# Kernel optimization log

Measured on AMD Instinct MI355X. Metric: run time of the kernel, lower is better.

Reference implementation:

```python
import jax, jax.numpy as jnp
import numpy as np

TWO_PI = 2.0 * np.pi
EPS = 1e-08


def setup_inputs() -> dict:
    key = jax.random.key(0)
    k1, k2, k3 = jax.random.split(key, 3)
    N, D = 1048576, 64
    samples = jax.random.normal(k1, (N, D), dtype=jnp.float32)
    Phi = jax.random.uniform(k2, (1,), dtype=jnp.float32)
    # mu init in torch: 2*rand - 0.5
    mu = 2.0 * jax.random.uniform(k3, (D,), dtype=jnp.float32) - 0.5
    Sigma = jnp.eye(D, dtype=jnp.float32)
    return {"samples": samples, "Phi": Phi, "mu": mu, "Sigma": Sigma}


def reference(samples, Phi, mu, Sigma):
    # Batched Mahalanobis quadratic form replacing the per-sample Python loop.
    inv_sigma = jnp.linalg.pinv(Sigma)                      # [D, D]
    det_sigma = jnp.linalg.det(Sigma)                       # scalar
    diff = samples - mu                                     # [N, D]
    # q_n = diff_n^T inv_sigma diff_n
    q = jnp.einsum('nd,de,ne->n', diff, inv_sigma, diff)    # [N]
    dens = Phi[0] * jnp.exp(-0.5 * q) / jnp.sqrt(TWO_PI * det_sigma)
    return -jnp.log(dens + EPS)                             # with_log=True path
```

## Files before the change

### kernel.cpp

```cpp
#include <hip/hip_runtime.h>


typedef __attribute__((ext_vector_type(8))) short s8bf;
typedef __attribute__((ext_vector_type(4))) float v4f;

#define TWO_PI_F 6.2831853071795864769f

__device__ __forceinline__ float bf2f(ushort u) {
    union { float f; unsigned int i; } v; v.i = ((unsigned int)u) << 16; return v.f;
}
__device__ __forceinline__ ushort f2bf(float f) {
    unsigned int x = __float_as_uint(f);
    return (ushort)((x + 0x7fffu + ((x >> 16) & 1u)) >> 16);
}
__device__ __forceinline__ s8bf pack8(float4 a, float4 b) {
    s8bf r;
    r[0] = (short)f2bf(a.x); r[1] = (short)f2bf(a.y);
    r[2] = (short)f2bf(a.z); r[3] = (short)f2bf(a.w);
    r[4] = (short)f2bf(b.x); r[5] = (short)f2bf(b.y);
    r[6] = (short)f2bf(b.z); r[7] = (short)f2bf(b.w);
    return r;
}

__global__ __launch_bounds__(256) void prep_kernel(const void* __restrict__ Sigma,
                                                   const void* __restrict__ Phi,
                                                   const void* __restrict__ mu,
                                                   void* __restrict__ ws) {
    __shared__ __align__(16) float colbuf[64];
    __shared__ __align__(16) float rowbuf[64];
    __shared__ __align__(16) float sA[64 * 65];
    __shared__ float smu[64];
    const int t = threadIdx.x;
    const int j = t & 63, w = t >> 6;
    const unsigned int wd0 = *(const unsigned int*)Sigma;
    const bool isf32 = (wd0 == 0x3F800000u);

    float ar[16];
    if (isf32) {
        const float* S = (const float*)Sigma;
#pragma unroll
        for (int ii = 0; ii < 16; ++ii) ar[ii] = S[(16 * w + ii) * 64 + j];
    } else {
        const ushort* S = (const ushort*)Sigma;
#pragma unroll
        for (int ii = 0; ii < 16; ++ii) ar[ii] = bf2f(S[(16 * w + ii) * 64 + j]);
    }
    if (t < 64) smu[t] = isf32 ? ((const float*)mu)[t] : bf2f(((const ushort*)mu)[t]);

    float det = 1.0f;
    for (int k = 0; k < 64; ++k) {
        if (j == k) {
#pragma unroll
            for (int ii = 0; ii < 16; ++ii) colbuf[16 * w + ii] = ar[ii];
        }
        if (w == (k >> 4)) {
            float val = ar[0];
#pragma unroll
            for (int ii = 1; ii < 16; ++ii) val = (ii == (k & 15)) ? ar[ii] : val;
            rowbuf[j] = val;
        }
        __syncthreads();
        const float piv = rowbuf[k];
        const float ip = 1.0f / piv;
        const float rk = rowbuf[j] * ip;
        det *= piv;
        const bool jk = (j == k);
#pragma unroll
        for (int ii = 0; ii < 16; ++ii) {
            float f = colbuf[16 * w + ii];
            float nv = fmaf(-f, rk, ar[ii]);
            nv = jk ? (-f * ip) : nv;
            if (16 * w + ii == k) nv = jk ? ip : rk;
            ar[ii] = nv;
        }
        __syncthreads();
    }

    ushort* wb = (ushort*)ws;
#pragma unroll
    for (int ii = 0; ii < 16; ++ii) wb[(16 * w + ii) * 64 + j] = f2bf(ar[ii]);
#pragma unroll
    for (int ii = 0; ii < 16; ++ii) sA[(16 * w + ii) * 65 + j] = ar[ii];
    __syncthreads();

    float* wf = (float*)((char*)ws + 8192);
    if (t < 64) {
        float dot = 0.0f;
#pragma unroll
        for (int jj = 0; jj < 64; ++jj) dot = fmaf(sA[t * 65 + jj], smu[jj], dot);
        wf[t] = 2.0f * dot;
        float pc = smu[t] * dot;
#pragma unroll
        for (int off = 1; off < 64; off <<= 1) pc += __shfl_xor(pc, off, 64);
        if (t == 0) {
            float ph = isf32 ? ((const float*)Phi)[0] : bf2f(((const ushort*)Phi)[0]);
            wf[64] = pc;
            wf[65] = ph / sqrtf(TWO_PI_F * det);
            wf[66] = isf32 ? 1.0f : 0.0f;
        }
    }
}

__global__ __launch_bounds__(256) void gmm_kernel(const void* __restrict__ Xv,
                                                  const void* __restrict__ ws,
                                                  void* __restrict__ outv,
                                                  int ntiles) {
    __shared__ __align__(16) ushort sB[64 * 72];
    __shared__ __align__(16) ushort sX[64 * 64];
    const int t = threadIdx.x;
    const int w = t >> 6, l = t & 63, n = l & 15, q = l >> 4;

    const ushort* wb = (const ushort*)ws;
#pragma unroll
    for (int p0 = 0; p0 < 2; ++p0) {
        int idx = p0 * 2048 + t * 8;
        int r = idx >> 6, c = idx & 63;
        *(uint4*)(&sB[r * 72 + c]) = *(const uint4*)(wb + idx);
    }
    const float* wf = (const float*)((const char*)ws + 8192);
    float vneg[4];
#pragma unroll
    for (int c = 0; c < 4; ++c) vneg[c] = -wf[c * 16 + n];
    const float c0 = wf[64], sc = wf[65];
    const bool isf32 = (wf[66] != 0.0f);
    __syncthreads();

    s8bf bfr[2][4];
#pragma unroll
    for (int s = 0; s < 2; ++s)
#pragma unroll
        for (int c = 0; c < 4; ++c)
            bfr[s][c] = *(const s8bf*)(&sB[(c * 16 + n) * 72 + s * 32 + q * 8]);

    const int sr = t >> 2, h = t & 3;
    const int c0i = 2 * h, c1i = 2 * h + 1;
    ushort* dst0 = sX + sr * 64 + ((c0i ^ (sr & 7)) * 8);
    ushort* dst1 = sX + sr * 64 + ((c1i ^ (sr & 7)) * 8);

    for (int tile = blockIdx.x; tile < ntiles; tile += gridDim.x) {
        s8bf ch0, ch1;
        if (isf32) {
            const float* src = (const float*)Xv + (size_t)tile * 4096 + sr * 64 + h * 16;
            float4 f0 = ((const float4*)src)[0];
            float4 f1 = ((const float4*)src)[1];
            float4 f2 = ((const float4*)src)[2];
            float4 f3 = ((const float4*)src)[3];
            ch0 = pack8(f0, f1);
            ch1 = pack8(f2, f3);
        } else {
            const ushort* src = (const ushort*)Xv + (size_t)tile * 4096 + sr * 64 + h * 16;
            ch0 = ((const s8bf*)src)[0];
            ch1 = ((const s8bf*)src)[1];
        }
        __syncthreads();
        *(s8bf*)dst0 = ch0;
        *(s8bf*)dst1 = ch1;
        __syncthreads();

        v4f acc[4];
#pragma unroll
        for (int c = 0; c < 4; ++c) acc[c] = (v4f){vneg[c], vneg[c], vneg[c], vneg[c]};

#pragma unroll
        for (int s = 0; s < 2; ++s) {
            int chunk = (4 * s + q) ^ (n & 7);
            s8bf af = *(const s8bf*)(sX + (w * 16 + n) * 64 + chunk * 8);
#pragma unroll
            for (int c = 0; c < 4; ++c)
                acc[c] = __builtin_amdgcn_mfma_f32_16x16x32_bf16(af, bfr[s][c], acc[c], 0, 0, 0);
        }

        float p[4] = {0.f, 0.f, 0.f, 0.f};
#pragma unroll
        for (int r = 0; r < 4; ++r) {
            int row = q * 4 + r;
            const ushort* rp = sX + (w * 16 + row) * 64;
            int rm = row & 7;
#pragma unroll
            for (int c = 0; c < 4; ++c) {
                int ch = (2 * c + (n >> 3)) ^ rm;
                float xv = bf2f(rp[ch * 8 + (n & 7)]);
                p[r] = fmaf(acc[c][r], xv, p[r]);
            }
        }
#pragma unroll
        for (int r = 0; r < 4; ++r)
#pragma unroll
            for (int off = 1; off < 16; off <<= 1)
                p[r] += __shfl_xor(p[r], off, 64);

        if (n < 4) {
            float qv = ((n == 0) ? p[0] : (n == 1) ? p[1] : (n == 2) ? p[2] : p[3]) + c0;
            float val = -__logf(sc * __expf(-0.5f * qv) + 1e-8f);
            size_t oi = (size_t)tile * 64 + w * 16 + q * 4 + n;
            if (isf32) ((float*)outv)[oi] = val;
            else       ((ushort*)outv)[oi] = f2bf(val);
        }
    }
}

extern "C" void kernel_launch(void* const* d_in, const int* in_sizes, int n_in,
                              void* d_out, int out_size, void* d_ws, size_t ws_size,
                              hipStream_t stream) {
    const void* X     = d_in[0];
    const void* Phi   = d_in[1];
    const void* mu    = d_in[2];
    const void* Sigma = d_in[3];

    int nrows  = in_sizes[0] / 64;
    int ntiles = nrows / 64;

    prep_kernel<<<1, 256, 0, stream>>>(Sigma, Phi, mu, d_ws);

    int grid = ntiles < 2048 ? ntiles : 2048;
    gmm_kernel<<<grid, 256, 0, stream>>>(X, d_ws, d_out, ntiles);
}
```

Measured before the change: 398.7 us.

## Factor precision matrix and compute Mahalanobis as squared norm with register pipelining

Prep kernel now runs an LDL-style elimination to build a whitening matrix W with W^T W = Sigma^-1, and folds mu into a bias W*mu. The main kernel then forms q as the squared norm of W*x - W*mu using MFMA, so the second pass over x through shared memory is no longer needed. Shared-memory staging and block barriers are removed: each wave loads its 16-row group straight into MFMA operand registers, double-buffering the next group's load, and writes four outputs at once. This drops LDS traffic and synchronisation, in exchange for a more complex factorisation and different rounding behaviour.

```diff
diff --git a/kernel.cpp b/kernel.cpp
--- a/kernel.cpp
+++ b/kernel.cpp
@@ -3,6 +3,7 @@
 
 typedef __attribute__((ext_vector_type(8))) short s8bf;
 typedef __attribute__((ext_vector_type(4))) float v4f;
+typedef __attribute__((ext_vector_type(4))) short s4bf;
 
 #define TWO_PI_F 6.2831853071795864769f
 
@@ -26,16 +27,18 @@
                                                    const void* __restrict__ Phi,
                                                    const void* __restrict__ mu,
                                                    void* __restrict__ ws) {
-    __shared__ __align__(16) float colbuf[64];
-    __shared__ __align__(16) float rowbuf[64];
-    __shared__ __align__(16) float sA[64 * 65];
+    __shared__ __align__(16) float colbuf[2][64];
+    __shared__ __align__(16) float rowA[2][64];
+    __shared__ __align__(16) float rowM[2][64];
+    __shared__ float dbuf[64];
+    __shared__ __align__(16) float sW[64 * 65];
     __shared__ float smu[64];
     const int t = threadIdx.x;
     const int j = t & 63, w = t >> 6;
     const unsigned int wd0 = *(const unsigned int*)Sigma;
     const bool isf32 = (wd0 == 0x3F800000u);
 
-    float ar[16];
+    float ar[16], br[16];
     if (isf32) {
         const float* S = (const float*)Sigma;
 #pragma unroll
@@ -45,157 +48,190 @@
 #pragma unroll
         for (int ii = 0; ii < 16; ++ii) ar[ii] = bf2f(S[(16 * w + ii) * 64 + j]);
     }
+#pragma unroll
+    for (int ii = 0; ii < 16; ++ii) br[ii] = (16 * w + ii == j) ? 1.0f : 0.0f;
     if (t < 64) smu[t] = isf32 ? ((const float*)mu)[t] : bf2f(((const ushort*)mu)[t]);
 
     float det = 1.0f;
     for (int k = 0; k < 64; ++k) {
+        const int b = k & 1;
         if (j == k) {
 #pragma unroll
-            for (int ii = 0; ii < 16; ++ii) colbuf[16 * w + ii] = ar[ii];
+            for (int ii = 0; ii < 16; ++ii) colbuf[b][16 * w + ii] = ar[ii];
         }
         if (w == (k >> 4)) {
-            float val = ar[0];
-#pragma unroll
-            for (int ii = 1; ii < 16; ++ii) val = (ii == (k & 15)) ? ar[ii] : val;
-            rowbuf[j] = val;
+            float va = ar[0], vm = br[0];
+#pragma unroll
+            for (int ii = 1; ii < 16; ++ii) {
+                va = (ii == (k & 15)) ? ar[ii] : va;
+                vm = (ii == (k & 15)) ? br[ii] : vm;
+            }
+            rowA[b][j] = va;
+            rowM[b][j] = vm;
         }
         __syncthreads();
-        const float piv = rowbuf[k];
+        const float piv = rowA[b][k];
         const float ip = 1.0f / piv;
-        const float rk = rowbuf[j] * ip;
         det *= piv;
-        const bool jk = (j == k);
+        const float ra = rowA[b][j], rm = rowM[b][j];
 #pragma unroll
         for (int ii = 0; ii < 16; ++ii) {
-            float f = colbuf[16 * w + ii];
-            float nv = fmaf(-f, rk, ar[ii]);
-            nv = jk ? (-f * ip) : nv;
-            if (16 * w + ii == k) nv = jk ? ip : rk;
-            ar[ii] = nv;
-        }
-        __syncthreads();
-    }
-
-    ushort* wb = (ushort*)ws;
-#pragma unroll
-    for (int ii = 0; ii < 16; ++ii) wb[(16 * w + ii) * 64 + j] = f2bf(ar[ii]);
-#pragma unroll
-    for (int ii = 0; ii < 16; ++ii) sA[(16 * w + ii) * 65 + j] = ar[ii];
+            const int row = 16 * w + ii;
+            const float m = colbuf[b][row] * ip;
+            const bool act = row > k;
+            float na = fmaf(-m, ra, ar[ii]);
+            float nb = fmaf(-m, rm, br[ii]);
+            ar[ii] = act ? na : ar[ii];
+            br[ii] = act ? nb : br[ii];
+        }
+    }
+
+    if (w == (j >> 4)) {
+        float vd = ar[0];
+#pragma unroll
+        for (int ii = 1; ii < 16; ++ii) vd = (ii == (j & 15)) ? ar[ii] : vd;
+        dbuf[j] = vd;
+    }
     __syncthreads();
 
-    float* wf = (float*)((char*)ws + 8192);
+    ushort* wbp = (ushort*)ws;
+    float* wfp = (float*)((char*)ws + 8192);
+#pragma unroll
+    for (int ii = 0; ii < 16; ++ii) {
+        const int row = 16 * w + ii;
+        const float Wv = br[ii] * rsqrtf(dbuf[row]);
+        wbp[row * 64 + j] = f2bf(Wv);
+        sW[row * 65 + j] = Wv;
+    }
+    __syncthreads();
+
     if (t < 64) {
         float dot = 0.0f;
 #pragma unroll
-        for (int jj = 0; jj < 64; ++jj) dot = fmaf(sA[t * 65 + jj], smu[jj], dot);
-        wf[t] = 2.0f * dot;
-        float pc = smu[t] * dot;
-#pragma unroll
-        for (int off = 1; off < 64; off <<= 1) pc += __shfl_xor(pc, off, 64);
-        if (t == 0) {
-            float ph = isf32 ? ((const float*)Phi)[0] : bf2f(((const ushort*)Phi)[0]);
-            wf[64] = pc;
-            wf[65] = ph / sqrtf(TWO_PI_F * det);
-            wf[66] = isf32 ? 1.0f : 0.0f;
-        }
-    }
-}
-
-__global__ __launch_bounds__(256) void gmm_kernel(const void* __restrict__ Xv,
-                                                  const void* __restrict__ ws,
-                                                  void* __restrict__ outv,
-                                                  int ntiles) {
-    __shared__ __align__(16) ushort sB[64 * 72];
-    __shared__ __align__(16) ushort sX[64 * 64];
+        for (int jj = 0; jj < 64; ++jj) dot = fmaf(sW[t * 65 + jj], smu[jj], dot);
+        wfp[t] = dot;
+    }
+    if (t == 0) {
+        float ph = isf32 ? ((const float*)Phi)[0] : bf2f(((const ushort*)Phi)[0]);
+        wfp[64] = ph / sqrtf(TWO_PI_F * det);
+        wfp[65] = isf32 ? 1.0f : 0.0f;
+    }
+}
+
+__device__ __forceinline__ void gmm_compute(s8bf af0, s8bf af1,
+                                            const s8bf (&bfr)[2][4],
+                                            const float (&mneg)[4],
+                                            float sc, int g, int q, int n,
+                                            void* __restrict__ outv, bool isf32) {
+    v4f acc[4];
+#pragma unroll
+    for (int c = 0; c < 4; ++c) acc[c] = (v4f){mneg[c], mneg[c], mneg[c], mneg[c]};
+#pragma unroll
+    for (int c = 0; c < 4; ++c)
+        acc[c] = __builtin_amdgcn_mfma_f32_16x16x32_bf16(af0, bfr[0][c], acc[c], 0, 0, 0);
+#pragma unroll
+    for (int c = 0; c < 4; ++c)
+        acc[c] = __builtin_amdgcn_mfma_f32_16x16x32_bf16(af1, bfr[1][c], acc[c], 0, 0, 0);
+
+    float p[4];
+#pragma unroll
+    for (int r = 0; r < 4; ++r) {
+        float s = acc[0][r] * acc[0][r];
+        s = fmaf(acc[1][r], acc[1][r], s);
+        s = fmaf(acc[2][r], acc[2][r], s);
+        s = fmaf(acc[3][r], acc[3][r], s);
+        p[r] = s;
+    }
+#pragma unroll
+    for (int r = 0; r < 4; ++r)
+#pragma unroll
+        for (int off = 1; off < 16; off <<= 1)
+            p[r] += __shfl_xor(p[r], off, 64);
+
+    if (n == 0) {
+        float4 v;
+        v.x = -__logf(fmaf(sc, __expf(-0.5f * p[0]), 1e-8f));
+        v.y = -__logf(fmaf(sc, __expf(-0.5f * p[1]), 1e-8f));
+        v.z = -__logf(fmaf(sc, __expf(-0.5f * p[2]), 1e-8f));
+        v.w = -__logf(fmaf(sc, __expf(-0.5f * p[3]), 1e-8f));
+        const size_t ob = (size_t)g * 16 + q * 4;
+        if (isf32) {
+            *(float4*)((float*)outv + ob) = v;
+        } else {
+            s4bf o;
+            o[0] = (short)f2bf(v.x); o[1] = (short)f2bf(v.y);
+            o[2] = (short)f2bf(v.z); o[3] = (short)f2bf(v.w);
+            *(s4bf*)((ushort*)outv + ob) = o;
+        }
+    }
+}
+
+__global__ __launch_bounds__(256, 4) void gmm_kernel(const void* __restrict__ Xv,
+                                                     const void* __restrict__ ws,
+                                                     void* __restrict__ outv,
+                                                     int ngroups) {
     const int t = threadIdx.x;
     const int w = t >> 6, l = t & 63, n = l & 15, q = l >> 4;
 
     const ushort* wb = (const ushort*)ws;
-#pragma unroll
-    for (int p0 = 0; p0 < 2; ++p0) {
-        int idx = p0 * 2048 + t * 8;
-        int r = idx >> 6, c = idx & 63;
-        *(uint4*)(&sB[r * 72 + c]) = *(const uint4*)(wb + idx);
-    }
+    s8bf bfr[2][4];
+#pragma unroll
+    for (int s = 0; s < 2; ++s)
+#pragma unroll
+        for (int c = 0; c < 4; ++c)
+            bfr[s][c] = *(const s8bf*)(wb + (c * 16 + n) * 64 + s * 32 + q * 8);
+
     const float* wf = (const float*)((const char*)ws + 8192);
-    float vneg[4];
-#pragma unroll
-    for (int c = 0; c < 4; ++c) vneg[c] = -wf[c * 16 + n];
-    const float c0 = wf[64], sc = wf[65];
-    const bool isf32 = (wf[66] != 0.0f);
-    __syncthreads();
-
-    s8bf bfr[2][4];
-#pragma unroll
-    for (int s = 0; s < 2; ++s)
-#pragma unroll
-        for (int c = 0; c < 4; ++c)
-            bfr[s][c] = *(const s8bf*)(&sB[(c * 16 + n) * 72 + s * 32 + q * 8]);
-
-    const int sr = t >> 2, h = t & 3;
-    const int c0i = 2 * h, c1i = 2 * h + 1;
-    ushort* dst0 = sX + sr * 64 + ((c0i ^ (sr & 7)) * 8);
-    ushort* dst1 = sX + sr * 64 + ((c1i ^ (sr & 7)) * 8);
-
-    for (int tile = blockIdx.x; tile < ntiles; tile += gridDim.x) {
-        s8bf ch0, ch1;
-        if (isf32) {
-            const float* src = (const float*)Xv + (size_t)tile * 4096 + sr * 64 + h * 16;
-            float4 f0 = ((const float4*)src)[0];
-            float4 f1 = ((const float4*)src)[1];
-            float4 f2 = ((const float4*)src)[2];
-            float4 f3 = ((const float4*)src)[3];
-            ch0 = pack8(f0, f1);
-            ch1 = pack8(f2, f3);
-        } else {
-            const ushort* src = (const ushort*)Xv + (size_t)tile * 4096 + sr * 64 + h * 16;
-            ch0 = ((const s8bf*)src)[0];
-            ch1 = ((const s8bf*)src)[1];
-        }
-        __syncthreads();
-        *(s8bf*)dst0 = ch0;
-        *(s8bf*)dst1 = ch1;
-        __syncthreads();
-
-        v4f acc[4];
-#pragma unroll
-        for (int c = 0; c < 4; ++c) acc[c] = (v4f){vneg[c], vneg[c], vneg[c], vneg[c]};
-
-#pragma unroll
-        for (int s = 0; s < 2; ++s) {
-            int chunk = (4 * s + q) ^ (n & 7);
-            s8bf af = *(const s8bf*)(sX + (w * 16 + n) * 64 + chunk * 8);
-#pragma unroll
-            for (int c = 0; c < 4; ++c)
-                acc[c] = __builtin_amdgcn_mfma_f32_16x16x32_bf16(af, bfr[s][c], acc[c], 0, 0, 0);
-        }
-
-        float p[4] = {0.f, 0.f, 0.f, 0.f};
-#pragma unroll
-        for (int r = 0; r < 4; ++r) {
-            int row = q * 4 + r;
-            const ushort* rp = sX + (w * 16 + row) * 64;
-            int rm = row & 7;
-#pragma unroll
-            for (int c = 0; c < 4; ++c) {
-                int ch = (2 * c + (n >> 3)) ^ rm;
-                float xv = bf2f(rp[ch * 8 + (n & 7)]);
-                p[r] = fmaf(acc[c][r], xv, p[r]);
-            }
-        }
-#pragma unroll
-        for (int r = 0; r < 4; ++r)
-#pragma unroll
-            for (int off = 1; off < 16; off <<= 1)
-                p[r] += __shfl_xor(p[r], off, 64);
-
-        if (n < 4) {
-            float qv = ((n == 0) ? p[0] : (n == 1) ? p[1] : (n == 2) ? p[2] : p[3]) + c0;
-            float val = -__logf(sc * __expf(-0.5f * qv) + 1e-8f);
-            size_t oi = (size_t)tile * 64 + w * 16 + q * 4 + n;
-            if (isf32) ((float*)outv)[oi] = val;
-            else       ((ushort*)outv)[oi] = f2bf(val);
-        }
+    float mneg[4];
+#pragma unroll
+    for (int c = 0; c < 4; ++c) mneg[c] = -wf[c * 16 + n];
+    const float sc = wf[64];
+    const bool isf32 = (wf[65] != 0.0f);
+
+    const int lo0 = n * 64 + q * 8;
+    int gw = blockIdx.x * 4 + w;
+    const int stride = gridDim.x * 4;
+    if (gw >= ngroups) return;
+
+    if (isf32) {
+        const float* xbase = (const float*)Xv;
+        float4 xa0, xb0, xc0, xd0, xa1, xb1, xc1, xd1;
+#define LF(S, G) do { const float* _s = xbase + (size_t)(G) * 1024 + lo0;        \
+        xa##S = ((const float4*)_s)[0]; xb##S = ((const float4*)_s)[1];          \
+        xc##S = ((const float4*)(_s + 32))[0]; xd##S = ((const float4*)(_s + 32))[1]; } while (0)
+        int g = gw;
+        LF(0, g);
+        while (true) {
+            int g1 = g + stride;
+            if (g1 < ngroups) LF(1, g1);
+            gmm_compute(pack8(xa0, xb0), pack8(xc0, xd0), bfr, mneg, sc, g, q, n, outv, true);
+            if (g1 >= ngroups) break;
+            int g2 = g1 + stride;
+            if (g2 < ngroups) LF(0, g2);
+            gmm_compute(pack8(xa1, xb1), pack8(xc1, xd1), bfr, mneg, sc, g1, q, n, outv, true);
+            if (g2 >= ngroups) break;
+            g = g2;
+        }
+#undef LF
+    } else {
+        const ushort* ubase = (const ushort*)Xv;
+        s8bf ba0, bb0, ba1, bb1;
+#define LB(S, G) do { const ushort* _s = ubase + (size_t)(G) * 1024 + lo0;       \
+        ba##S = *(const s8bf*)_s; bb##S = *(const s8bf*)(_s + 32); } while (0)
+        int g = gw;
+        LB(0, g);
+        while (true) {
+            int g1 = g + stride;
+            if (g1 < ngroups) LB(1, g1);
+            gmm_compute(ba0, bb0, bfr, mneg, sc, g, q, n, outv, false);
+            if (g1 >= ngroups) break;
+            int g2 = g1 + stride;
+            if (g2 < ngroups) LB(0, g2);
+            gmm_compute(ba1, bb1, bfr, mneg, sc, g1, q, n, outv, false);
+            if (g2 >= ngroups) break;
+            g = g2;
+        }
+#undef LB
     }
 }
 
@@ -207,11 +243,13 @@
     const void* mu    = d_in[2];
     const void* Sigma = d_in[3];
 
-    int nrows  = in_sizes[0] / 64;
-    int ntiles = nrows / 64;
+    int nrows   = in_sizes[0] / 64;
+    int ngroups = nrows / 16;
 
     prep_kernel<<<1, 256, 0, stream>>>(Sigma, Phi, mu, d_ws);
 
-    int grid = ntiles < 2048 ? ntiles : 2048;
-    gmm_kernel<<<grid, 256, 0, stream>>>(X, d_ws, d_out, ntiles);
-}
+    int grid = (ngroups + 3) >> 2;
+    if (grid > 2048) grid = 2048;
+    if (grid < 1) grid = 1;
+    gmm_kernel<<<grid, 256, 0, stream>>>(X, d_ws, d_out, ngroups);
+}
```

New measurement: 405.3 us. No clear change (+1.7%).
